# Kernel tuning notes

Measured on AMD Instinct MI355X. Metric: run time of the kernel, lower is better.

Reference implementation:

```python
import jax, jax.numpy as jnp
import numpy as np

H, I, QKV, TV = 2048, 8192, 8192, 4096
NVH, NKH, KD, VD, KC = 32, 16, 128, 128, 4

def _rms(x, w, eps=1e-6):
    # [x,-x]->LayerNorm trick: doubled mean is 0, so it reduces to x*rsqrt(mean(x^2)+eps)
    return x * jax.lax.rsqrt(jnp.mean(x * x, -1, keepdims=True) + eps) * (1.0 + w)

def _silu(x):
    return x * jax.nn.sigmoid(x)

def setup_inputs() -> dict:
    key = jax.random.key(0)
    ks = jax.random.split(key, 16)
    w = lambda i, shape, s=0.02: jax.random.normal(ks[i], shape, jnp.float32) * s
    return {
        'x': jax.random.normal(ks[0], (1, H), jnp.float32),
        'conv_state': jax.random.normal(ks[1], (QKV, KC), jnp.float32) * 0.1,
        'ssm_state': jax.random.normal(ks[2], (NVH, KD, VD), jnp.float32) * 0.1,
        'in_proj_w': w(3, (QKV + TV + 2 * NVH, H)),
        'out_proj_w': w(4, (H, TV)),
        'conv_weight': w(5, (QKV, KC), 0.5),
        'A_log': w(6, (NVH,), 0.1),
        'dt_bias': w(7, (NVH,), 0.1),
        'norm_weight': jnp.ones((VD,), jnp.float32),
        'rms1_w': w(8, (H,)),
        'rms2_w': w(9, (H,)),
        'gate_w': w(10, (I, H)),
        'up_w': w(11, (I, H)),
        'down_w': w(12, (H, I)),
    }

def reference(x, conv_state, ssm_state, in_proj_w, out_proj_w, conv_weight,
              A_log, dt_bias, norm_weight, rms1_w, rms2_w, gate_w, up_w, down_w):
    residual = x  # [1, H]
    h = _rms(x, rms1_w)
    proj = h @ in_proj_w.T  # [1, QKV+TV+2*NVH]
    mixed_qkv = proj[:, :QKV]
    z = proj[:, QKV:QKV + TV]
    a_raw = proj[0, QKV + TV:QKV + TV + NVH]
    b_raw = proj[0, QKV + TV + NVH:]

    # causal conv step: shift state, append new token, depthwise conv + silu
    new_conv_state = jnp.concatenate([conv_state[:, 1:], mixed_qkv[0][:, None]], axis=1)  # [QKV, KC]
    conv_out = _silu(jnp.sum(new_conv_state * conv_weight, axis=1))  # [QKV]

    KT = NKH * KD
    q = conv_out[:KT].reshape(NKH, KD)
    k = conv_out[KT:2 * KT].reshape(NKH, KD)
    v = conv_out[2 * KT:].reshape(NVH, VD)
    ratio = NVH // NKH
    q = jnp.repeat(q, ratio, axis=0)  # [NVH, KD]
    k = jnp.repeat(k, ratio, axis=0)
    l2 = lambda t: t / jnp.maximum(jnp.linalg.norm(t, axis=-1, keepdims=True), 1e-12)
    q = l2(q) * (KD ** -0.5)
    k = l2(k)

    beta = jax.nn.sigmoid(b_raw)  # [NVH]
    g = -jnp.exp(A_log) * jax.nn.softplus(a_raw + dt_bias)
    decay = jnp.exp(g)  # [NVH]

    # delta-rule fast-weight update
    decayed = decay[:, None, None] * ssm_state  # [NVH, KD, VD]
    Sk = jnp.einsum('hkv,hk->hv', decayed, k)
    delta = (v - Sk) * beta[:, None]
    new_ssm = decayed + k[:, :, None] * delta[:, None, :]
    y = jnp.einsum('hkv,hk->hv', new_ssm, q)  # [NVH, VD]

    # doubled-LayerNorm (eps=1e-6) with direct weight (not 1+w)
    y_n = y * jax.lax.rsqrt(jnp.mean(y * y, -1, keepdims=True) + 1e-6) * norm_weight
    y_out = (y_n * _silu(z.reshape(NVH, VD))).reshape(1, -1)  # [1, TV]
    attn_out = y_out @ out_proj_w.T
    x1 = residual + attn_out

    h2 = _rms(x1, rms2_w)
    ffn = (_silu(h2 @ gate_w.T) * (h2 @ up_w.T)) @ down_w.T
    return (x1 + ffn, new_conv_state, new_ssm)
```

## Files before the change

kernel.cpp:

```cpp
#include <hip/hip_runtime.h>
#include <math.h>

#define HD    2048
#define QKVD  8192
#define TVD   4096
#define NVHD  32
#define NKHD  16
#define KDD   128
#define VDD   128
#define PROJN (QKVD + TVD + 2*NVHD)

__device__ __forceinline__ float sigmoidf_(float x) { return 1.0f / (1.0f + expf(-x)); }
__device__ __forceinline__ float siluf_(float x)    { return x / (1.0f + expf(-x)); }
__device__ __forceinline__ float softplusf_(float x){ return (x > 20.0f) ? x : log1pf(expf(x)); }

__device__ __forceinline__ float waveReduceSum(float v) {
#pragma unroll
    for (int o = 32; o > 0; o >>= 1) v += __shfl_down(v, o, 64);
    return v;
}

__device__ __forceinline__ float blockReduceSum256(float v, float* red) {
    const int lane = threadIdx.x & 63, wid = threadIdx.x >> 6;
    v = waveReduceSum(v);
    if (lane == 0) red[wid] = v;
    __syncthreads();
    float s = red[0] + red[1] + red[2] + red[3];
    __syncthreads();
    return s;
}

__global__ void k0_rms1(const float* __restrict__ x, const float* __restrict__ w1,
                        float* __restrict__ hvec, float* __restrict__ ss2) {
    __shared__ float red[4];
    const int t = threadIdx.x;
    float s = 0.f;
#pragma unroll
    for (int i = t; i < HD/4; i += 256) {
        float4 v = ((const float4*)x)[i];
        s += v.x*v.x + v.y*v.y + v.z*v.z + v.w*v.w;
    }
    s = blockReduceSum256(s, red);
    const float r = rsqrtf(s / (float)HD + 1e-6f);
#pragma unroll
    for (int i = t; i < HD/4; i += 256) {
        float4 v = ((const float4*)x)[i];
        float4 w = ((const float4*)w1)[i];
        float4 o = make_float4(v.x*r*(1.f+w.x), v.y*r*(1.f+w.y),
                               v.z*r*(1.f+w.z), v.w*r*(1.f+w.w));
        ((float4*)hvec)[i] = o;
    }
    if (t == 0) *ss2 = 0.f;
}

template<int COLS>
__global__ void gemv_rows(const float* __restrict__ W, const float* __restrict__ v,
                          float* __restrict__ out) {
    const int wid = threadIdx.x >> 6, lane = threadIdx.x & 63;
    const int row = blockIdx.x * 4 + wid;
    const float4* Wr = (const float4*)(W + (size_t)row * COLS);
    const float4* vr = (const float4*)v;
    float acc = 0.f;
#pragma unroll
    for (int i = 0; i < COLS/256; i++) {
        float4 a = Wr[lane + i*64];
        float4 b = vr[lane + i*64];
        acc += a.x*b.x + a.y*b.y + a.z*b.z + a.w*b.w;
    }
    acc = waveReduceSum(acc);
    if (lane == 0) out[row] = acc;
}

__global__ void k2_ssm(const float* __restrict__ proj,
                       const float* __restrict__ conv_state,
                       const float* __restrict__ conv_weight,
                       const float* __restrict__ ssm_state,
                       const float* __restrict__ A_log,
                       const float* __restrict__ dt_bias,
                       const float* __restrict__ norm_weight,
                       float* __restrict__ new_conv_state,
                       float* __restrict__ new_ssm,
                       float* __restrict__ yout) {
    const int head  = blockIdx.x;
    const int t     = threadIdx.x;
    const int qhead = head >> 1;

    __shared__ float red[4];
    __shared__ float q_s[KDD], k_s[KDD], v_s[VDD];
    __shared__ float skr2[256], sqr2[256];

    float qv = 0.f, kv = 0.f, vv = 0.f;
    if (t < 128) {
        int cq = qhead*KDD + t;
        float4 cs = *(const float4*)(conv_state + (size_t)cq*4);
        float4 w  = *(const float4*)(conv_weight + (size_t)cq*4);
        float xm  = proj[cq];
        qv = siluf_(cs.y*w.x + cs.z*w.y + cs.w*w.z + xm*w.w);
        *(float4*)(new_conv_state + (size_t)cq*4) = make_float4(cs.y, cs.z, cs.w, xm);
        int ck = 2048 + qhead*KDD + t;
        cs = *(const float4*)(conv_state + (size_t)ck*4);
        w  = *(const float4*)(conv_weight + (size_t)ck*4);
        xm = proj[ck];
        kv = siluf_(cs.y*w.x + cs.z*w.y + cs.w*w.z + xm*w.w);
        *(float4*)(new_conv_state + (size_t)ck*4) = make_float4(cs.y, cs.z, cs.w, xm);
        int cv = 4096 + head*VDD + t;
        cs = *(const float4*)(conv_state + (size_t)cv*4);
        w  = *(const float4*)(conv_weight + (size_t)cv*4);
        xm = proj[cv];
        vv = siluf_(cs.y*w.x + cs.z*w.y + cs.w*w.z + xm*w.w);
        *(float4*)(new_conv_state + (size_t)cv*4) = make_float4(cs.y, cs.z, cs.w, xm);
    }

    const float sq = blockReduceSum256(qv*qv, red);
    const float sk = blockReduceSum256(kv*kv, red);
    const float qn = qv / fmaxf(sqrtf(sq), 1e-12f) * 0.08838834764831845f;
    const float kn = kv / fmaxf(sqrtf(sk), 1e-12f);
    const float kq = blockReduceSum256(qn*kn, red);

    if (t < 128) { q_s[t] = qn; k_s[t] = kn; v_s[t] = vv; }
    __syncthreads();

    const float a_raw = proj[QKVD + TVD + head];
    const float b_raw = proj[QKVD + TVD + NVHD + head];
    const float beta  = sigmoidf_(b_raw);
    const float g     = -expf(A_log[head]) * softplusf_(a_raw + dt_bias[head]);
    const float decay = expf(g);

    const int col = t & 127;
    const int kh  = t >> 7;
    const float* Sp = ssm_state + (size_t)head*KDD*VDD + (size_t)kh*64*VDD + col;
    float skr = 0.f, sqr = 0.f;
#pragma unroll 16
    for (int k = 0; k < 64; k++) {
        float s = Sp[k*VDD];
        skr += s * k_s[kh*64 + k];
        sqr += s * q_s[kh*64 + k];
    }
    skr2[t] = skr; sqr2[t] = sqr;
    __syncthreads();
    const float Skr = skr2[col] + skr2[col + 128];
    const float Sqr = sqr2[col] + sqr2[col + 128];
    const float delta = (v_s[col] - decay * Skr) * beta;

    float* Np = new_ssm + (size_t)head*KDD*VDD + (size_t)kh*64*VDD + col;
#pragma unroll 16
    for (int k = 0; k < 64; k++) {
        float s = Sp[k*VDD];
        Np[k*VDD] = decay * s + k_s[kh*64 + k] * delta;
    }

    const float y = decay * Sqr + delta * kq;
    const float sy = blockReduceSum256((kh == 0) ? y*y : 0.f, red);
    if (t < 128) {
        const float r  = rsqrtf(sy / (float)VDD + 1e-6f);
        const float z  = proj[QKVD + head*VDD + t];
        yout[head*VDD + t] = y * r * norm_weight[t] * siluf_(z);
    }
}

__global__ void k3_outproj(const float* __restrict__ W, const float* __restrict__ yout,
                           const float* __restrict__ x, float* __restrict__ x1,
                           float* __restrict__ ss2) {
    __shared__ float part[4];
    const int wid = threadIdx.x >> 6, lane = threadIdx.x & 63;
    const int row = blockIdx.x * 4 + wid;
    const float4* Wr = (const float4*)(W + (size_t)row * TVD);
    const float4* vr = (const float4*)yout;
    float acc = 0.f;
#pragma unroll
    for (int i = 0; i < TVD/256; i++) {
        float4 a = Wr[lane + i*64];
        float4 b = vr[lane + i*64];
        acc += a.x*b.x + a.y*b.y + a.z*b.z + a.w*b.w;
    }
    acc = waveReduceSum(acc);
    if (lane == 0) {
        float xv = x[row] + acc;
        x1[row] = xv;
        part[wid] = xv * xv;
    }
    __syncthreads();
    if (threadIdx.x == 0) atomicAdd(ss2, part[0] + part[1] + part[2] + part[3]);
}

__global__ void k4_gateup(const float* __restrict__ GW, const float* __restrict__ UW,
                          const float* __restrict__ x1, const float* __restrict__ w2,
                          const float* __restrict__ ss2, float* __restrict__ m) {
    const int wid = threadIdx.x >> 6, lane = threadIdx.x & 63;
    const int row = blockIdx.x * 4 + wid;
    const float r = rsqrtf(*ss2 / (float)HD + 1e-6f);
    const float4* Gr = (const float4*)(GW + (size_t)row * HD);
    const float4* Ur = (const float4*)(UW + (size_t)row * HD);
    const float4* xr = (const float4*)x1;
    const float4* wr = (const float4*)w2;
    float ag = 0.f, au = 0.f;
#pragma unroll
    for (int i = 0; i < HD/256; i++) {
        float4 xv = xr[lane + i*64];
        float4 wv = wr[lane + i*64];
        float4 tt = make_float4(xv.x*(1.f+wv.x), xv.y*(1.f+wv.y),
                                xv.z*(1.f+wv.z), xv.w*(1.f+wv.w));
        float4 gv = Gr[lane + i*64];
        float4 uv = Ur[lane + i*64];
        ag += gv.x*tt.x + gv.y*tt.y + gv.z*tt.z + gv.w*tt.w;
        au += uv.x*tt.x + uv.y*tt.y + uv.z*tt.z + uv.w*tt.w;
    }
    ag = waveReduceSum(ag);
    au = waveReduceSum(au);
    if (lane == 0) {
        ag *= r; au *= r;
        m[row] = siluf_(ag) * au;
    }
}

__global__ void k5_down(const float* __restrict__ W, const float* __restrict__ m,
                        const float* __restrict__ x1, float* __restrict__ out0) {
    const int wid = threadIdx.x >> 6, lane = threadIdx.x & 63;
    const int row = blockIdx.x * 4 + wid;
    const float4* Wr = (const float4*)(W + (size_t)row * 8192);
    const float4* vr = (const float4*)m;
    float acc = 0.f;
#pragma unroll 8
    for (int i = 0; i < 8192/256; i++) {
        float4 a = Wr[lane + i*64];
        float4 b = vr[lane + i*64];
        acc += a.x*b.x + a.y*b.y + a.z*b.z + a.w*b.w;
    }
    acc = waveReduceSum(acc);
    if (lane == 0) out0[row] = x1[row] + acc;
}

extern "C" void kernel_launch(void* const* d_in, const int* in_sizes, int n_in,
                              void* d_out, int out_size, void* d_ws, size_t ws_size,
                              hipStream_t stream) {
    const float* x           = (const float*)d_in[0];
    const float* conv_state  = (const float*)d_in[1];
    const float* ssm_state   = (const float*)d_in[2];
    const float* in_proj_w   = (const float*)d_in[3];
    const float* out_proj_w  = (const float*)d_in[4];
    const float* conv_weight = (const float*)d_in[5];
    const float* A_log       = (const float*)d_in[6];
    const float* dt_bias     = (const float*)d_in[7];
    const float* norm_weight = (const float*)d_in[8];
    const float* rms1_w      = (const float*)d_in[9];
    const float* rms2_w      = (const float*)d_in[10];
    const float* gate_w      = (const float*)d_in[11];
    const float* up_w        = (const float*)d_in[12];
    const float* down_w      = (const float*)d_in[13];

    float* out0          = (float*)d_out;
    float* new_conv      = out0 + HD;
    float* new_ssm       = new_conv + QKVD*4;

    float* ws   = (float*)d_ws;
    float* hvec = ws;
    float* proj = hvec + HD;
    float* yout = proj + PROJN;
    float* x1   = yout + TVD;
    float* ss2  = x1 + HD;
    float* mmid = ss2 + 4;

    k0_rms1<<<1, 256, 0, stream>>>(x, rms1_w, hvec, ss2);
    gemv_rows<HD><<<PROJN/4, 256, 0, stream>>>(in_proj_w, hvec, proj);
    k2_ssm<<<NVHD, 256, 0, stream>>>(proj, conv_state, conv_weight, ssm_state,
                                     A_log, dt_bias, norm_weight,
                                     new_conv, new_ssm, yout);
    k3_outproj<<<HD/4, 256, 0, stream>>>(out_proj_w, yout, x, x1, ss2);
    k4_gateup<<<8192/4, 256, 0, stream>>>(gate_w, up_w, x1, rms2_w, ss2, mmid);
    k5_down<<<HD/4, 256, 0, stream>>>(down_w, mmid, x1, out0);
}
```

Before: 336.9 us.

## Fuse RMSNorms into GEMV kernels, add nontemporal loads, rebalance SSM and row splits

Folds the first RMSNorm into the in-projection GEMV, with every block recomputing the norm into shared memory, and moves the second RMSNorm into the gate/up kernel. This drops one launch and the atomic sum-of-squares reduction. Weight streams now use nontemporal loads. The out-projection and down GEMVs use one row per block split across four waves, and the SSM kernel runs 512 threads per head with 32 k-rows per thread group. The cost is redundant norm computation in every block and more blocks for the row-split GEMVs.

```diff
diff --git a/kernel.cpp b/kernel.cpp
--- a/kernel.cpp
+++ b/kernel.cpp
@@ -10,9 +10,13 @@
 #define VDD   128
 #define PROJN (QKVD + TVD + 2*NVHD)
 
+typedef float f4 __attribute__((ext_vector_type(4)));
+
 __device__ __forceinline__ float sigmoidf_(float x) { return 1.0f / (1.0f + expf(-x)); }
 __device__ __forceinline__ float siluf_(float x)    { return x / (1.0f + expf(-x)); }
 __device__ __forceinline__ float softplusf_(float x){ return (x > 20.0f) ? x : log1pf(expf(x)); }
+__device__ __forceinline__ float dot4(f4 a, f4 b)   { return a.x*b.x + a.y*b.y + a.z*b.z + a.w*b.w; }
+__device__ __forceinline__ f4 ntload(const f4* p)   { return __builtin_nontemporal_load(p); }
 
 __device__ __forceinline__ float waveReduceSum(float v) {
 #pragma unroll
@@ -20,58 +24,56 @@
     return v;
 }
 
-__device__ __forceinline__ float blockReduceSum256(float v, float* red) {
+template<int NW>
+__device__ __forceinline__ float blockReduceSum(float v, float* red) {
     const int lane = threadIdx.x & 63, wid = threadIdx.x >> 6;
     v = waveReduceSum(v);
     if (lane == 0) red[wid] = v;
     __syncthreads();
-    float s = red[0] + red[1] + red[2] + red[3];
+    float s = 0.f;
+#pragma unroll
+    for (int w = 0; w < NW; w++) s += red[w];
     __syncthreads();
     return s;
 }
 
-__global__ void k0_rms1(const float* __restrict__ x, const float* __restrict__ w1,
-                        float* __restrict__ hvec, float* __restrict__ ss2) {
+__global__ void kA_inproj(const float* __restrict__ x, const float* __restrict__ w1,
+                          const float* __restrict__ W, float* __restrict__ proj) {
     __shared__ float red[4];
+    __shared__ float hl[HD];
     const int t = threadIdx.x;
+
+    f4 xv[2];
     float s = 0.f;
 #pragma unroll
-    for (int i = t; i < HD/4; i += 256) {
-        float4 v = ((const float4*)x)[i];
-        s += v.x*v.x + v.y*v.y + v.z*v.z + v.w*v.w;
-    }
-    s = blockReduceSum256(s, red);
+    for (int i = 0; i < 2; i++) {
+        xv[i] = ((const f4*)x)[t + i*256];
+        s += dot4(xv[i], xv[i]);
+    }
+    s = blockReduceSum<4>(s, red);
     const float r = rsqrtf(s / (float)HD + 1e-6f);
 #pragma unroll
-    for (int i = t; i < HD/4; i += 256) {
-        float4 v = ((const float4*)x)[i];
-        float4 w = ((const float4*)w1)[i];
-        float4 o = make_float4(v.x*r*(1.f+w.x), v.y*r*(1.f+w.y),
-                               v.z*r*(1.f+w.z), v.w*r*(1.f+w.w));
-        ((float4*)hvec)[i] = o;
-    }
-    if (t == 0) *ss2 = 0.f;
-}
-
-template<int COLS>
-__global__ void gemv_rows(const float* __restrict__ W, const float* __restrict__ v,
-                          float* __restrict__ out) {
-    const int wid = threadIdx.x >> 6, lane = threadIdx.x & 63;
+    for (int i = 0; i < 2; i++) {
+        f4 wv = ((const f4*)w1)[t + i*256];
+        ((f4*)hl)[t + i*256] = xv[i] * r * (wv + 1.0f);
+    }
+    __syncthreads();
+
+    const int wid = t >> 6, lane = t & 63;
     const int row = blockIdx.x * 4 + wid;
-    const float4* Wr = (const float4*)(W + (size_t)row * COLS);
-    const float4* vr = (const float4*)v;
+    const f4* Wr = (const f4*)(W + (size_t)row * HD);
     float acc = 0.f;
 #pragma unroll
-    for (int i = 0; i < COLS/256; i++) {
-        float4 a = Wr[lane + i*64];
-        float4 b = vr[lane + i*64];
-        acc += a.x*b.x + a.y*b.y + a.z*b.z + a.w*b.w;
+    for (int i = 0; i < 8; i++) {
+        f4 a = ntload(&Wr[lane + i*64]);
+        f4 b = ((const f4*)hl)[lane + i*64];
+        acc += dot4(a, b);
     }
     acc = waveReduceSum(acc);
-    if (lane == 0) out[row] = acc;
-}
-
-__global__ void k2_ssm(const float* __restrict__ proj,
+    if (lane == 0) proj[row] = acc;
+}
+
+__global__ void kB_ssm(const float* __restrict__ proj,
                        const float* __restrict__ conv_state,
                        const float* __restrict__ conv_weight,
                        const float* __restrict__ ssm_state,
@@ -85,37 +87,42 @@
     const int t     = threadIdx.x;
     const int qhead = head >> 1;
 
-    __shared__ float red[4];
+    __shared__ float red[8];
     __shared__ float q_s[KDD], k_s[KDD], v_s[VDD];
-    __shared__ float skr2[256], sqr2[256];
+    __shared__ float skr2[512], sqr2[512];
 
     float qv = 0.f, kv = 0.f, vv = 0.f;
     if (t < 128) {
         int cq = qhead*KDD + t;
-        float4 cs = *(const float4*)(conv_state + (size_t)cq*4);
-        float4 w  = *(const float4*)(conv_weight + (size_t)cq*4);
-        float xm  = proj[cq];
+        f4 cs = *(const f4*)(conv_state + (size_t)cq*4);
+        f4 w  = *(const f4*)(conv_weight + (size_t)cq*4);
+        float xm = proj[cq];
         qv = siluf_(cs.y*w.x + cs.z*w.y + cs.w*w.z + xm*w.w);
-        *(float4*)(new_conv_state + (size_t)cq*4) = make_float4(cs.y, cs.z, cs.w, xm);
+        f4 nc; nc.x = cs.y; nc.y = cs.z; nc.z = cs.w; nc.w = xm;
+        *(f4*)(new_conv_state + (size_t)cq*4) = nc;
+
         int ck = 2048 + qhead*KDD + t;
-        cs = *(const float4*)(conv_state + (size_t)ck*4);
-        w  = *(const float4*)(conv_weight + (size_t)ck*4);
+        cs = *(const f4*)(conv_state + (size_t)ck*4);
+        w  = *(const f4*)(conv_weight + (size_t)ck*4);
         xm = proj[ck];
         kv = siluf_(cs.y*w.x + cs.z*w.y + cs.w*w.z + xm*w.w);
-        *(float4*)(new_conv_state + (size_t)ck*4) = make_float4(cs.y, cs.z, cs.w, xm);
+        nc.x = cs.y; nc.y = cs.z; nc.z = cs.w; nc.w = xm;
+        *(f4*)(new_conv_state + (size_t)ck*4) = nc;
+
         int cv = 4096 + head*VDD + t;
-        cs = *(const float4*)(conv_state + (size_t)cv*4);
-        w  = *(const float4*)(conv_weight + (size_t)cv*4);
+        cs = *(const f4*)(conv_state + (size_t)cv*4);
+        w  = *(const f4*)(conv_weight + (size_t)cv*4);
         xm = proj[cv];
         vv = siluf_(cs.y*w.x + cs.z*w.y + cs.w*w.z + xm*w.w);
-        *(float4*)(new_conv_state + (size_t)cv*4) = make_float4(cs.y, cs.z, cs.w, xm);
-    }
-
-    const float sq = blockReduceSum256(qv*qv, red);
-    const float sk = blockReduceSum256(kv*kv, red);
+        nc.x = cs.y; nc.y = cs.z; nc.z = cs.w; nc.w = xm;
+        *(f4*)(new_conv_state + (size_t)cv*4) = nc;
+    }
+
+    const float sq = blockReduceSum<8>(qv*qv, red);
+    const float sk = blockReduceSum<8>(kv*kv, red);
     const float qn = qv / fmaxf(sqrtf(sq), 1e-12f) * 0.08838834764831845f;
     const float kn = kv / fmaxf(sqrtf(sk), 1e-12f);
-    const float kq = blockReduceSum256(qn*kn, red);
+    const float kq = blockReduceSum<8>(qn*kn, red);
 
     if (t < 128) { q_s[t] = qn; k_s[t] = kn; v_s[t] = vv; }
     __syncthreads();
@@ -128,82 +135,88 @@
 
     const int col = t & 127;
     const int kh  = t >> 7;
-    const float* Sp = ssm_state + (size_t)head*KDD*VDD + (size_t)kh*64*VDD + col;
+    const float* Sp = ssm_state + (size_t)head*KDD*VDD + (size_t)kh*32*VDD + col;
     float skr = 0.f, sqr = 0.f;
-#pragma unroll 16
-    for (int k = 0; k < 64; k++) {
-        float s = Sp[k*VDD];
-        skr += s * k_s[kh*64 + k];
-        sqr += s * q_s[kh*64 + k];
+#pragma unroll 8
+    for (int k = 0; k < 32; k++) {
+        float sv = Sp[k*VDD];
+        skr += sv * k_s[kh*32 + k];
+        sqr += sv * q_s[kh*32 + k];
     }
     skr2[t] = skr; sqr2[t] = sqr;
     __syncthreads();
-    const float Skr = skr2[col] + skr2[col + 128];
-    const float Sqr = sqr2[col] + sqr2[col + 128];
+    const float Skr = skr2[col] + skr2[col+128] + skr2[col+256] + skr2[col+384];
+    const float Sqr = sqr2[col] + sqr2[col+128] + sqr2[col+256] + sqr2[col+384];
     const float delta = (v_s[col] - decay * Skr) * beta;
 
-    float* Np = new_ssm + (size_t)head*KDD*VDD + (size_t)kh*64*VDD + col;
-#pragma unroll 16
-    for (int k = 0; k < 64; k++) {
-        float s = Sp[k*VDD];
-        Np[k*VDD] = decay * s + k_s[kh*64 + k] * delta;
+    float* Np = new_ssm + (size_t)head*KDD*VDD + (size_t)kh*32*VDD + col;
+#pragma unroll 8
+    for (int k = 0; k < 32; k++) {
+        float sv = Sp[k*VDD];
+        Np[k*VDD] = decay * sv + k_s[kh*32 + k] * delta;
     }
 
     const float y = decay * Sqr + delta * kq;
-    const float sy = blockReduceSum256((kh == 0) ? y*y : 0.f, red);
+    const float sy = blockReduceSum<8>((kh == 0) ? y*y : 0.f, red);
     if (t < 128) {
-        const float r  = rsqrtf(sy / (float)VDD + 1e-6f);
+        const float rr = rsqrtf(sy / (float)VDD + 1e-6f);
         const float z  = proj[QKVD + head*VDD + t];
-        yout[head*VDD + t] = y * r * norm_weight[t] * siluf_(z);
-    }
-}
-
-__global__ void k3_outproj(const float* __restrict__ W, const float* __restrict__ yout,
-                           const float* __restrict__ x, float* __restrict__ x1,
-                           float* __restrict__ ss2) {
+        yout[head*VDD + t] = y * rr * norm_weight[t] * siluf_(z);
+    }
+}
+
+__global__ void kC_outproj(const float* __restrict__ W, const float* __restrict__ y,
+                           const float* __restrict__ x, float* __restrict__ x1) {
     __shared__ float part[4];
-    const int wid = threadIdx.x >> 6, lane = threadIdx.x & 63;
+    const int t = threadIdx.x, wid = t >> 6, lane = t & 63;
+    const int row = blockIdx.x;
+    const f4* Wr = (const f4*)(W + (size_t)row * TVD);
+    const f4* vr = (const f4*)y;
+    float acc = 0.f;
+#pragma unroll
+    for (int i = 0; i < 4; i++) {
+        int idx = wid*256 + i*64 + lane;
+        acc += dot4(ntload(&Wr[idx]), vr[idx]);
+    }
+    acc = waveReduceSum(acc);
+    if (lane == 0) part[wid] = acc;
+    __syncthreads();
+    if (t == 0) x1[row] = x[row] + part[0] + part[1] + part[2] + part[3];
+}
+
+__global__ void kD_gateup(const float* __restrict__ GW, const float* __restrict__ UW,
+                          const float* __restrict__ x1, const float* __restrict__ w2,
+                          float* __restrict__ m) {
+    __shared__ float red[4];
+    __shared__ float tl[HD];
+    const int t = threadIdx.x;
+
+    f4 xv[2];
+    float s = 0.f;
+#pragma unroll
+    for (int i = 0; i < 2; i++) {
+        xv[i] = ((const f4*)x1)[t + i*256];
+        s += dot4(xv[i], xv[i]);
+    }
+    s = blockReduceSum<4>(s, red);
+    const float r = rsqrtf(s / (float)HD + 1e-6f);
+#pragma unroll
+    for (int i = 0; i < 2; i++) {
+        f4 wv = ((const f4*)w2)[t + i*256];
+        ((f4*)tl)[t + i*256] = xv[i] * (wv + 1.0f);
+    }
+    __syncthreads();
+
+    const int wid = t >> 6, lane = t & 63;
     const int row = blockIdx.x * 4 + wid;
-    const float4* Wr = (const float4*)(W + (size_t)row * TVD);
-    const float4* vr = (const float4*)yout;
-    float acc = 0.f;
-#pragma unroll
-    for (int i = 0; i < TVD/256; i++) {
-        float4 a = Wr[lane + i*64];
-        float4 b = vr[lane + i*64];
-        acc += a.x*b.x + a.y*b.y + a.z*b.z + a.w*b.w;
-    }
-    acc = waveReduceSum(acc);
-    if (lane == 0) {
-        float xv = x[row] + acc;
-        x1[row] = xv;
-        part[wid] = xv * xv;
-    }
-    __syncthreads();
-    if (threadIdx.x == 0) atomicAdd(ss2, part[0] + part[1] + part[2] + part[3]);
-}
-
-__global__ void k4_gateup(const float* __restrict__ GW, const float* __restrict__ UW,
-                          const float* __restrict__ x1, const float* __restrict__ w2,
-                          const float* __restrict__ ss2, float* __restrict__ m) {
-    const int wid = threadIdx.x >> 6, lane = threadIdx.x & 63;
-    const int row = blockIdx.x * 4 + wid;
-    const float r = rsqrtf(*ss2 / (float)HD + 1e-6f);
-    const float4* Gr = (const float4*)(GW + (size_t)row * HD);
-    const float4* Ur = (const float4*)(UW + (size_t)row * HD);
-    const float4* xr = (const float4*)x1;
-    const float4* wr = (const float4*)w2;
+    const f4* Gr = (const f4*)(GW + (size_t)row * HD);
+    const f4* Ur = (const f4*)(UW + (size_t)row * HD);
     float ag = 0.f, au = 0.f;
 #pragma unroll
-    for (int i = 0; i < HD/256; i++) {
-        float4 xv = xr[lane + i*64];
-        float4 wv = wr[lane + i*64];
-        float4 tt = make_float4(xv.x*(1.f+wv.x), xv.y*(1.f+wv.y),
-                                xv.z*(1.f+wv.z), xv.w*(1.f+wv.w));
-        float4 gv = Gr[lane + i*64];
-        float4 uv = Ur[lane + i*64];
-        ag += gv.x*tt.x + gv.y*tt.y + gv.z*tt.z + gv.w*tt.w;
-        au += uv.x*tt.x + uv.y*tt.y + uv.z*tt.z + uv.w*tt.w;
+    for (int i = 0; i < 8; i++) {
+        f4 tt = ((const f4*)tl)[lane + i*64];
+        ag += dot4(ntload(&Gr[lane + i*64]), tt);
+        au += dot4(ntload(&Ur[lane + i*64]), tt);
     }
     ag = waveReduceSum(ag);
     au = waveReduceSum(au);
@@ -213,21 +226,23 @@
     }
 }
 
-__global__ void k5_down(const float* __restrict__ W, const float* __restrict__ m,
+__global__ void kE_down(const float* __restrict__ W, const float* __restrict__ m,
                         const float* __restrict__ x1, float* __restrict__ out0) {
-    const int wid = threadIdx.x >> 6, lane = threadIdx.x & 63;
-    const int row = blockIdx.x * 4 + wid;
-    const float4* Wr = (const float4*)(W + (size_t)row * 8192);
-    const float4* vr = (const float4*)m;
+    __shared__ float part[4];
+    const int t = threadIdx.x, wid = t >> 6, lane = t & 63;
+    const int row = blockIdx.x;
+    const f4* Wr = (const f4*)(W + (size_t)row * 8192);
+    const f4* vr = (const f4*)m;
     float acc = 0.f;
-#pragma unroll 8
-    for (int i = 0; i < 8192/256; i++) {
-        float4 a = Wr[lane + i*64];
-        float4 b = vr[lane + i*64];
-        acc += a.x*b.x + a.y*b.y + a.z*b.z + a.w*b.w;
+#pragma unroll
+    for (int i = 0; i < 8; i++) {
+        int idx = wid*512 + i*64 + lane;
+        acc += dot4(ntload(&Wr[idx]), vr[idx]);
     }
     acc = waveReduceSum(acc);
-    if (lane == 0) out0[row] = x1[row] + acc;
+    if (lane == 0) part[wid] = acc;
+    __syncthreads();
+    if (t == 0) out0[row] = x1[row] + part[0] + part[1] + part[2] + part[3];
 }
 
 extern "C" void kernel_launch(void* const* d_in, const int* in_sizes, int n_in,
@@ -248,24 +263,21 @@
     const float* up_w        = (const float*)d_in[12];
     const float* down_w      = (const float*)d_in[13];
 
-    float* out0          = (float*)d_out;
-    float* new_conv      = out0 + HD;
-    float* new_ssm       = new_conv + QKVD*4;
+    float* out0     = (float*)d_out;
+    float* new_conv = out0 + HD;
+    float* new_ssm  = new_conv + QKVD*4;
 
     float* ws   = (float*)d_ws;
-    float* hvec = ws;
-    float* proj = hvec + HD;
+    float* proj = ws;
     float* yout = proj + PROJN;
     float* x1   = yout + TVD;
-    float* ss2  = x1 + HD;
-    float* mmid = ss2 + 4;
-
-    k0_rms1<<<1, 256, 0, stream>>>(x, rms1_w, hvec, ss2);
-    gemv_rows<HD><<<PROJN/4, 256, 0, stream>>>(in_proj_w, hvec, proj);
-    k2_ssm<<<NVHD, 256, 0, stream>>>(proj, conv_state, conv_weight, ssm_state,
+    float* mmid = x1 + HD;
+
+    kA_inproj<<<PROJN/4, 256, 0, stream>>>(x, rms1_w, in_proj_w, proj);
+    kB_ssm<<<NVHD, 512, 0, stream>>>(proj, conv_state, conv_weight, ssm_state,
                                      A_log, dt_bias, norm_weight,
                                      new_conv, new_ssm, yout);
-    k3_outproj<<<HD/4, 256, 0, stream>>>(out_proj_w, yout, x, x1, ss2);
-    k4_gateup<<<8192/4, 256, 0, stream>>>(gate_w, up_w, x1, rms2_w, ss2, mmid);
-    k5_down<<<HD/4, 256, 0, stream>>>(down_w, mmid, x1, out0);
-}
+    kC_outproj<<<HD, 256, 0, stream>>>(out_proj_w, yout, x, x1);
+    kD_gateup<<<8192/4, 256, 0, stream>>>(gate_w, up_w, x1, rms2_w, mmid);
+    kE_down<<<HD, 256, 0, stream>>>(down_w, mmid, x1, out0);
+}
```

New measurement: 311.3 us. 7.6% less time.
